# Kernel optimization log

Hardware: AMD Instinct MI355X
Metric: run time of the kernel (lower is better)

The kernel has to match this reference:

```python
import jax, jax.numpy as jnp
import numpy as np

T, B, A, OBS = 128, 16, 32, 256
K, NACT, HID = 3, 9, 32


def setup_inputs() -> dict:
    key = jax.random.key(0)
    ks = jax.random.split(key, 12)
    sc = 0.1  # small init scale for stability
    d = {}
    d["x"] = jax.random.normal(ks[0], (T, B, A, OBS), jnp.float32)
    d["done"] = jax.random.randint(ks[1], (T, B), 0, 2, jnp.int32)
    d["actions"] = jax.random.randint(ks[2], (T, B, A, K), 0, NACT, jnp.int32)
    d["W1"] = sc * jax.random.normal(ks[3], (128, OBS), jnp.float32)
    d["b1"] = jnp.zeros((128,), jnp.float32)
    d["W2"] = sc * jax.random.normal(ks[4], (128, 128), jnp.float32)
    d["b2"] = jnp.zeros((128,), jnp.float32)
    d["W3"] = sc * jax.random.normal(ks[5], (64, 128), jnp.float32)
    d["b3"] = jnp.zeros((64,), jnp.float32)
    d["Wih"] = sc * jax.random.normal(ks[6], (4 * HID, 64), jnp.float32)
    d["Whh"] = sc * jax.random.normal(ks[7], (4 * HID, HID), jnp.float32)
    d["bih"] = jnp.zeros((4 * HID,), jnp.float32)
    d["bhh"] = jnp.zeros((4 * HID,), jnp.float32)
    d["Wh"] = sc * jax.random.normal(ks[8], (K, NACT, HID), jnp.float32)
    d["bh"] = jnp.zeros((K, NACT), jnp.float32)
    d["h0"] = jnp.zeros((B * A, HID), jnp.float32)
    d["c0"] = jnp.zeros((B * A, HID), jnp.float32)
    return d


def _forward(x, done, actions, W1, b1, W2, b2, W3, b3,
             Wih, Whh, bih, bhh, Wh, bh, h0, c0):
    # MLP trunk: n_obs -> 128 -> 128 -> 64 (tanh, tanh, linear)
    z = jnp.tanh(x @ W1.T + b1)
    z = jnp.tanh(z @ W2.T + b2)
    z = z @ W3.T + b3                       # [T, B, A, 64]
    zf = z.reshape(T, B * A, 64)
    # done[t] repeated per agent (repeat_interleave along batch*agent axis)
    done_f = jnp.repeat(done.astype(x.dtype), A, axis=1)  # [T, B*A]

    def step(carry, inp):
        h, c = carry
        zt, dt = inp                        # [B*A,64], [B*A]
        mask = (1.0 - dt)[:, None]
        h = h * mask
        c = c * mask
        gates = zt @ Wih.T + bih + h @ Whh.T + bhh  # [B*A, 4H]
        i, f, g, o = jnp.split(gates, 4, axis=-1)   # PyTorch gate order i,f,g,o
        i, f, o = jax.nn.sigmoid(i), jax.nn.sigmoid(f), jax.nn.sigmoid(o)
        g = jnp.tanh(g)
        c = f * c + i * g
        h = o * jnp.tanh(c)
        return (h, c), h

    (_, _), ys = jax.lax.scan(step, (h0, c0), (zf, done_f))
    y = ys.reshape(T, B, A, HID)
    # multi-head categorical logits: stacked heads [K, NACT, HID]
    logits = jnp.einsum('tbah,knh->tbakn', y, Wh) + bh  # [T,B,A,K,NACT]
    lp = jax.nn.log_softmax(logits, axis=-1)
    entropies = -jnp.sum(jnp.exp(lp) * lp, axis=-1)     # [T,B,A,K]
    alp = jnp.take_along_axis(lp, actions[..., None], axis=-1)[..., 0]  # [T,B,A,K]
    logprobs = jnp.prod(alp, axis=-1)  # faithful: product of per-head log-probs
    return logprobs, entropies


def reference(x, done, actions, W1, b1, W2, b2, W3, b3,
              Wih, Whh, bih, bhh, Wh, bh, h0, c0):
    logprobs, entropies = _forward(x, done, actions, W1, b1, W2, b2, W3, b3,
                                   Wih, Whh, bih, bhh, Wh, bh, h0, c0)
    return actions, logprobs, entropies
```

## Files before the change

kernel.cpp:

```cpp
#include <hip/hip_runtime.h>
#include <math.h>

namespace {
constexpr int Tn = 128, Bn = 16, An = 32, OBS = 256, Kh = 3, NACT = 9, HID = 32;
constexpr int TBA = Tn * Bn * An;
constexpr int BA  = Bn * An;
constexpr int OUT_LP  = TBA * Kh;
constexpr int OUT_ENT = TBA * Kh + TBA;
constexpr int NCHUNK = 8;
constexpr int CHUNKW = Tn / NCHUNK;

constexpr int W1_OFF  = 0;
constexpr int W2_OFF  = 32768;
constexpr int W3_OFF  = 49152;
constexpr int WIH_OFF = 57344;
constexpr int W16_TOT = 65536;

typedef __fp16   pk16x2 __attribute__((ext_vector_type(2)));
typedef _Float16 half8v __attribute__((ext_vector_type(8)));
typedef float    f32x4  __attribute__((ext_vector_type(4)));
}

__device__ __forceinline__ float fast_sig(float x) {
  return __builtin_amdgcn_rcpf(1.f + __expf(-x));
}
__device__ __forceinline__ float fast_tanh(float x) {
  return fmaf(2.f, fast_sig(2.f * x), -1.f);
}
__device__ __forceinline__ unsigned h2bits(pk16x2 h) {
  return __builtin_bit_cast(unsigned, h);
}
__device__ __forceinline__ pk16x2 bits2h(unsigned u) {
  return __builtin_bit_cast(pk16x2, u);
}
__device__ __forceinline__ float dot2(pk16x2 a, pk16x2 b, float c) {
#if __has_builtin(__builtin_amdgcn_fdot2)
  return __builtin_amdgcn_fdot2(a, b, c, false);
#else
  c = fmaf((float)a.x, (float)b.x, c);
  return fmaf((float)a.y, (float)b.y, c);
#endif
}
__device__ __forceinline__ float dpp_swap1(float x) {
  return __uint_as_float((unsigned)__builtin_amdgcn_mov_dpp(
      (int)__float_as_uint(x), 0xB1, 0xF, 0xF, true));
}
__device__ __forceinline__ int first_done_ge(unsigned long long dm0,
                                             unsigned long long dm1, int n) {
  unsigned long long m0 = (n < 64) ? (dm0 & (~0ull << n)) : 0ull;
  unsigned long long m1 = (n < 64) ? dm1 : (dm1 & (~0ull << (n - 64)));
  if (m0) return __builtin_ctzll(m0);
  if (m1) return 64 + __builtin_ctzll(m1);
  return 128;
}

__global__ __launch_bounds__(256) void cvtw_act_kernel(
    const float* __restrict__ W1, const float* __restrict__ W2,
    const float* __restrict__ W3, const float* __restrict__ Wih,
    _Float16* __restrict__ w16, const int* __restrict__ actions,
    float* __restrict__ out)
{
  const int bid = blockIdx.x;
  if (bid < W16_TOT/256) {
    int i = bid * 256 + threadIdx.x;
    float v;
    if (i < W2_OFF)       v = W1[i];
    else if (i < W3_OFF)  v = W2[i - W2_OFF];
    else if (i < WIH_OFF) v = W3[i - W3_OFF];
    else                  v = Wih[i - WIH_OFF];
    w16[i] = (_Float16)v;
  } else {
    int i = (bid - W16_TOT/256) * 256 + threadIdx.x;
    out[i] = (float)actions[i];
  }
}

template<int ROWS, int WSTR>
__device__ __forceinline__ void stage_wh(const _Float16* __restrict__ Wg, int kofs,
                                         _Float16* __restrict__ wt, int tid)
{
#pragma unroll
  for (int it = 0; it < ROWS/64; ++it) {
    int idx = tid + it*512;
    int o = idx >> 3, g8 = idx & 7;
    *(half8v*)&wt[o*72 + g8*8] =
        *(const half8v*)&Wg[(size_t)o*WSTR + kofs + g8*8];
  }
}

template<int NOC, int XSTR>
__device__ __forceinline__ void mfma_slab(const _Float16* __restrict__ xsrc,
                                          const _Float16* __restrict__ wt,
                                          int rA, int ln, int quad, f32x4 acc[8])
{
#pragma unroll
  for (int kc = 0; kc < 2; ++kc) {
    half8v a = *(const half8v*)&xsrc[rA*XSTR + kc*32 + quad*8];
#pragma unroll
    for (int oc = 0; oc < NOC; ++oc) {
      half8v b = *(const half8v*)&wt[(oc*16 + ln)*72 + kc*32 + quad*8];
      acc[oc] = __builtin_amdgcn_mfma_f32_16x16x32_f16(a, b, acc[oc], 0, 0, 0);
    }
  }
}

__global__ __launch_bounds__(512) void mlp_kernel(
    const float* __restrict__ x, const _Float16* __restrict__ w16,
    const float* __restrict__ b1, const float* __restrict__ b2,
    const float* __restrict__ b3, const float* __restrict__ bih,
    const float* __restrict__ bhh, uint2* __restrict__ G1q)
{
  __shared__ __align__(16) _Float16 xs[128*72];
  __shared__ __align__(16) _Float16 wt[128*72];
  __shared__ __align__(16) _Float16 act[128*136];
  const _Float16* W1h  = w16 + W1_OFF;
  const _Float16* W2h  = w16 + W2_OFF;
  const _Float16* W3h  = w16 + W3_OFF;
  const _Float16* Wihh = w16 + WIH_OFF;
  const int tid  = threadIdx.x;
  const int w    = tid >> 6;
  const int lane = tid & 63;
  const int ln   = lane & 15;
  const int quad = lane >> 4;
  const int rA   = 16*w + ln;
  const int r0   = 16*w + quad*4;
  const int R0   = blockIdx.x * 128;
  f32x4 acc[8];

#pragma unroll
  for (int oc = 0; oc < 8; ++oc) acc[oc] = (f32x4)0.f;
  for (int kt = 0; kt < 4; ++kt) {
#pragma unroll
    for (int it = 0; it < 2; ++it) {
      int idx = tid + it*512;
      int r = idx >> 3, g8 = idx & 7;
      const float* xp = &x[(size_t)(R0 + r)*OBS + kt*64 + g8*8];
      float4 v0 = *(const float4*)xp;
      float4 v1 = *(const float4*)(xp + 4);
      half8v hv = { (_Float16)v0.x, (_Float16)v0.y, (_Float16)v0.z, (_Float16)v0.w,
                    (_Float16)v1.x, (_Float16)v1.y, (_Float16)v1.z, (_Float16)v1.w };
      *(half8v*)&xs[r*72 + g8*8] = hv;
    }
    stage_wh<128, 256>(W1h, kt*64, wt, tid);
    __syncthreads();
    mfma_slab<8, 72>(xs, wt, rA, ln, quad, acc);
    __syncthreads();
  }
#pragma unroll
  for (int oc = 0; oc < 8; ++oc) {
    int o = oc*16 + ln;
    float bv = b1[o];
#pragma unroll
    for (int r = 0; r < 4; ++r)
      act[(r0 + r)*136 + o] = (_Float16)fast_tanh(acc[oc][r] + bv);
  }

#pragma unroll
  for (int oc = 0; oc < 8; ++oc) acc[oc] = (f32x4)0.f;
  for (int kt = 0; kt < 2; ++kt) {
    stage_wh<128, 128>(W2h, kt*64, wt, tid);
    __syncthreads();
    mfma_slab<8, 136>(act + kt*64, wt, rA, ln, quad, acc);
    __syncthreads();
  }
#pragma unroll
  for (int oc = 0; oc < 8; ++oc) {
    int o = oc*16 + ln;
    float bv = b2[o];
#pragma unroll
    for (int r = 0; r < 4; ++r)
      act[(r0 + r)*136 + o] = (_Float16)fast_tanh(acc[oc][r] + bv);
  }

#pragma unroll
  for (int oc = 0; oc < 4; ++oc) acc[oc] = (f32x4)0.f;
  for (int kt = 0; kt < 2; ++kt) {
    stage_wh<64, 128>(W3h, kt*64, wt, tid);
    __syncthreads();
    mfma_slab<4, 136>(act + kt*64, wt, rA, ln, quad, acc);
    __syncthreads();
  }
#pragma unroll
  for (int oc = 0; oc < 4; ++oc) {
    int o = oc*16 + ln;
    float bv = b3[o];
#pragma unroll
    for (int r = 0; r < 4; ++r)
      xs[(r0 + r)*72 + o] = (_Float16)(acc[oc][r] + bv);
  }

#pragma unroll
  for (int oc = 0; oc < 8; ++oc) acc[oc] = (f32x4)0.f;
  stage_wh<128, 64>(Wihh, 0, wt, tid);
  __syncthreads();
  mfma_slab<8, 72>(xs, wt, rA, ln, quad, acc);
#pragma unroll
  for (int p = 0; p < 2; ++p) {
    int ui = p*16 + ln;
    float bi = bih[ui]      + bhh[ui];
    float bf = bih[ui + 32] + bhh[ui + 32];
    float bg = bih[ui + 64] + bhh[ui + 64];
    float bo = bih[ui + 96] + bhh[ui + 96];
#pragma unroll
    for (int r = 0; r < 4; ++r) {
      int n = R0 + r0 + r;
      uint2 q;
      q.x = h2bits(__builtin_amdgcn_cvt_pkrtz(acc[p  ][r] + bi, acc[p+4][r] + bg));
      q.y = h2bits(__builtin_amdgcn_cvt_pkrtz(acc[p+2][r] + bf, acc[p+6][r] + bo));
      G1q[(size_t)n*32 + ui] = q;
    }
  }
}

__global__ __launch_bounds__(64) void lstm_kernel(
    const uint2* __restrict__ G1q, const float* __restrict__ Whh,
    const int* __restrict__ done, const float* __restrict__ h0,
    const float* __restrict__ c0, unsigned* __restrict__ Y16)
{
  static_assert(BA == 512 && NCHUNK == 8, "index math below assumes 512x8");
  const int lane = threadIdx.x;
  const int u    = lane & 31;
  const int half = lane >> 5;
  const int row  = blockIdx.x & (BA - 1);
  const int ck   = blockIdx.x >> 9;
  const int b    = row >> 5;

  unsigned long long dm0 = __ballot(done[lane*Bn + b] != 0);
  unsigned long long dm1 = __ballot(done[(lane + 64)*Bn + b] != 0);

  const int s = (ck == 0) ? 0 : first_done_ge(dm0, dm1, ck * CHUNKW);
  const int e = (ck == NCHUNK - 1) ? Tn
                                   : first_done_ge(dm0, dm1, (ck + 1) * CHUNKW);
  if (s >= e) return;

  pk16x2 wA[16], wB[16];
  const int rwA = u + half*32;
#pragma unroll
  for (int k4 = 0; k4 < 8; ++k4) {
    float4 a  = *(const float4*)&Whh[(rwA     )*HID + k4*4];
    float4 bq = *(const float4*)&Whh[(rwA + 64)*HID + k4*4];
    wA[2*k4+0] = __builtin_amdgcn_cvt_pkrtz(a.x,  a.y);
    wA[2*k4+1] = __builtin_amdgcn_cvt_pkrtz(a.z,  a.w);
    wB[2*k4+0] = __builtin_amdgcn_cvt_pkrtz(bq.x, bq.y);
    wB[2*k4+1] = __builtin_amdgcn_cvt_pkrtz(bq.z, bq.w);
  }

  float c, h;
  if (ck == 0) { c = c0[row*HID + u]; h = h0[row*HID + u]; }
  else         { c = 0.f;             h = 0.f; }
  unsigned pk = h2bits(__builtin_amdgcn_cvt_pkrtz(h, dpp_swap1(h)));

  const float sSc = half ? 1.f : 2.f;
  const float m1c = half ? 1.f : 2.f;
  const float m0c = half ? 0.f : -1.f;

  const unsigned* gb = (const unsigned*)G1q + ((size_t)row*32 + u)*2 + half;
  const size_t gstride = (size_t)BA * 64;

  unsigned qcur = gb[(size_t)s * gstride];
  for (int t = s; t < e; ++t) {
    int tn = t + 1; tn = (tn < e) ? tn : (e - 1);
    unsigned qnext = gb[(size_t)tn * gstride];

    unsigned long long dbit = (t < 64) ? (dm0 >> t) : (dm1 >> (t - 64));
    float m = (dbit & 1ull) ? 0.f : 1.f;
    unsigned hp[16];
#pragma unroll
    for (int k = 0; k < 16; ++k)
      hp[k] = __builtin_amdgcn_readlane(pk, 2*k);
    float aA0 = 0.f, aA1 = 0.f, aB0 = 0.f, aB1 = 0.f;
#pragma unroll
    for (int k = 0; k < 16; k += 2) {
      pk16x2 ha = bits2h(hp[k]), hb = bits2h(hp[k+1]);
      aA0 = dot2(wA[k], ha, aA0); aA1 = dot2(wA[k+1], hb, aA1);
      aB0 = dot2(wB[k], ha, aB0); aB1 = dot2(wB[k+1], hb, aB1);
    }
    pk16x2 g2 = bits2h(qcur);
    float x0 = fmaf(m, aA0 + aA1, (float)g2.x);
    float x1 = fmaf(m, aB0 + aB1, (float)g2.y);
    float v0 = fast_sig(x0);
    float v1 = fmaf(m1c, fast_sig(sSc * x1), m0c);
    float o0 = __shfl_xor(v0, 32, 64);
    float o1 = __shfl_xor(v1, 32, 64);
    float iv = half ? o0 : v0;
    float fv = half ? v0 : o0;
    float gv = half ? o1 : v1;
    float ov = half ? v1 : o1;
    c = fmaf(fv, m * c, iv * gv);
    h = ov * fast_tanh(c);
    pk = h2bits(__builtin_amdgcn_cvt_pkrtz(h, dpp_swap1(h)));
    if ((lane & 33) == 0)
      Y16[((size_t)t*BA + row)*16 + (u >> 1)] = pk;

    qcur = qnext;
  }
}

__global__ __launch_bounds__(256) void head_kernel(
    const unsigned* __restrict__ Y16, const float* __restrict__ Wh,
    const float* __restrict__ bh, const int* __restrict__ actions,
    float* __restrict__ out)
{
  __shared__ __align__(16) float whs[27*32];
  __shared__ float bhs[32];
  const int tid = threadIdx.x;
  const int R0 = blockIdx.x * 256;
  for (int i = tid; i < 27*32; i += 256) whs[i] = Wh[i];
  if (tid < 27) bhs[tid] = bh[tid];
  const int row = R0 + tid;
  float yv[32];
#pragma unroll
  for (int i4 = 0; i4 < 4; ++i4) {
    uint4 yw = *(const uint4*)&Y16[(size_t)row*16 + i4*4];
    pk16x2 p0 = bits2h(yw.x), p1 = bits2h(yw.y), p2 = bits2h(yw.z), p3 = bits2h(yw.w);
    yv[i4*8+0] = (float)p0.x; yv[i4*8+1] = (float)p0.y;
    yv[i4*8+2] = (float)p1.x; yv[i4*8+3] = (float)p1.y;
    yv[i4*8+4] = (float)p2.x; yv[i4*8+5] = (float)p2.y;
    yv[i4*8+6] = (float)p3.x; yv[i4*8+7] = (float)p3.y;
  }
  __syncthreads();
  float l[27];
#pragma unroll
  for (int m = 0; m < 27; ++m) {
    float a = bhs[m];
#pragma unroll
    for (int k4 = 0; k4 < 8; ++k4) {
      float4 w4 = *(const float4*)&whs[m*32 + k4*4];
      a = fmaf(yv[k4*4+0], w4.x, a);
      a = fmaf(yv[k4*4+1], w4.y, a);
      a = fmaf(yv[k4*4+2], w4.z, a);
      a = fmaf(yv[k4*4+3], w4.w, a);
    }
    l[m] = a;
  }
  float logprob = 1.0f;
#pragma unroll
  for (int kk = 0; kk < 3; ++kk) {
    float mx = l[kk*9];
#pragma unroll
    for (int n = 1; n < 9; ++n) mx = fmaxf(mx, l[kk*9+n]);
    float s = 0.f;
#pragma unroll
    for (int n = 0; n < 9; ++n) s += __expf(l[kk*9+n] - mx);
    float lse = mx + __logf(s);
    float ent = 0.f;
#pragma unroll
    for (int n = 0; n < 9; ++n) {
      float lp = l[kk*9+n] - lse;
      ent -= __expf(lp) * lp;
    }
    int a = actions[row*3 + kk];
    float alp = 0.f;
#pragma unroll
    for (int n = 0; n < 9; ++n) alp = (a == n) ? (l[kk*9+n] - lse) : alp;
    logprob *= alp;
    out[OUT_ENT + row*3 + kk] = ent;
  }
  out[OUT_LP + row] = logprob;
}

extern "C" void kernel_launch(void* const* d_in, const int* in_sizes, int n_in,
                              void* d_out, int out_size, void* d_ws, size_t ws_size,
                              hipStream_t stream)
{
  const float* x       = (const float*)d_in[0];
  const int*   done    = (const int*)  d_in[1];
  const int*   actions = (const int*)  d_in[2];
  const float* W1  = (const float*)d_in[3];
  const float* b1  = (const float*)d_in[4];
  const float* W2  = (const float*)d_in[5];
  const float* b2  = (const float*)d_in[6];
  const float* W3  = (const float*)d_in[7];
  const float* b3  = (const float*)d_in[8];
  const float* Wih = (const float*)d_in[9];
  const float* Whh = (const float*)d_in[10];
  const float* bih = (const float*)d_in[11];
  const float* bhh = (const float*)d_in[12];
  const float* Wh  = (const float*)d_in[13];
  const float* bh  = (const float*)d_in[14];
  const float* h0  = (const float*)d_in[15];
  const float* c0  = (const float*)d_in[16];
  float* out = (float*)d_out;

  uint2* G1q = (uint2*)d_ws;
  unsigned* Y16 = (unsigned*)(G1q + (size_t)TBA*32);
  _Float16* W16 = (_Float16*)(Y16 + (size_t)TBA*16);

  cvtw_act_kernel<<<W16_TOT/256 + (TBA*Kh)/256, 256, 0, stream>>>(
      W1, W2, W3, Wih, W16, actions, out);
  mlp_kernel<<<TBA/128, 512, 0, stream>>>(x, W16, b1, b2, b3, bih, bhh, G1q);
  lstm_kernel<<<BA * NCHUNK, 64, 0, stream>>>(G1q, Whh, done, h0, c0, Y16);
  head_kernel<<<TBA/256, 256, 0, stream>>>(Y16, Wh, bh, actions, out);
}
```

Baseline: 172.4 us.

## Deepen LSTM gate prefetch, interleave gate lanes for DPP, double time chunks

```diff
diff --git a/kernel.cpp b/kernel.cpp
--- a/kernel.cpp
+++ b/kernel.cpp
@@ -7,7 +7,7 @@
 constexpr int BA  = Bn * An;
 constexpr int OUT_LP  = TBA * Kh;
 constexpr int OUT_ENT = TBA * Kh + TBA;
-constexpr int NCHUNK = 8;
+constexpr int NCHUNK = 16;
 constexpr int CHUNKW = Tn / NCHUNK;
 
 constexpr int W1_OFF  = 0;
@@ -44,6 +44,10 @@
 __device__ __forceinline__ float dpp_swap1(float x) {
   return __uint_as_float((unsigned)__builtin_amdgcn_mov_dpp(
       (int)__float_as_uint(x), 0xB1, 0xF, 0xF, true));
+}
+__device__ __forceinline__ float dpp_quad2(float x) {
+  return __uint_as_float((unsigned)__builtin_amdgcn_mov_dpp(
+      (int)__float_as_uint(x), 0x4E, 0xF, 0xF, true));
 }
 __device__ __forceinline__ int first_done_ge(unsigned long long dm0,
                                              unsigned long long dm1, int n) {
@@ -217,10 +221,10 @@
     const int* __restrict__ done, const float* __restrict__ h0,
     const float* __restrict__ c0, unsigned* __restrict__ Y16)
 {
-  static_assert(BA == 512 && NCHUNK == 8, "index math below assumes 512x8");
+  static_assert(BA == 512 && NCHUNK == 16, "index math below assumes 512x16");
   const int lane = threadIdx.x;
-  const int u    = lane & 31;
-  const int half = lane >> 5;
+  const int u    = lane >> 1;
+  const int half = lane & 1;
   const int row  = blockIdx.x & (BA - 1);
   const int ck   = blockIdx.x >> 9;
   const int b    = row >> 5;
@@ -248,52 +252,76 @@
   float c, h;
   if (ck == 0) { c = c0[row*HID + u]; h = h0[row*HID + u]; }
   else         { c = 0.f;             h = 0.f; }
-  unsigned pk = h2bits(__builtin_amdgcn_cvt_pkrtz(h, dpp_swap1(h)));
+  unsigned pk = h2bits(__builtin_amdgcn_cvt_pkrtz(h, dpp_quad2(h)));
 
   const float sSc = half ? 1.f : 2.f;
   const float m1c = half ? 1.f : 2.f;
   const float m0c = half ? 0.f : -1.f;
 
-  const unsigned* gb = (const unsigned*)G1q + ((size_t)row*32 + u)*2 + half;
+  const unsigned* gb = (const unsigned*)G1q + (size_t)row*64 + lane;
   const size_t gstride = (size_t)BA * 64;
 
-  unsigned qcur = gb[(size_t)s * gstride];
-  for (int t = s; t < e; ++t) {
-    int tn = t + 1; tn = (tn < e) ? tn : (e - 1);
-    unsigned qnext = gb[(size_t)tn * gstride];
-
-    unsigned long long dbit = (t < 64) ? (dm0 >> t) : (dm1 >> (t - 64));
-    float m = (dbit & 1ull) ? 0.f : 1.f;
-    unsigned hp[16];
-#pragma unroll
-    for (int k = 0; k < 16; ++k)
-      hp[k] = __builtin_amdgcn_readlane(pk, 2*k);
-    float aA0 = 0.f, aA1 = 0.f, aB0 = 0.f, aB1 = 0.f;
-#pragma unroll
-    for (int k = 0; k < 16; k += 2) {
-      pk16x2 ha = bits2h(hp[k]), hb = bits2h(hp[k+1]);
-      aA0 = dot2(wA[k], ha, aA0); aA1 = dot2(wA[k+1], hb, aA1);
-      aB0 = dot2(wB[k], ha, aB0); aB1 = dot2(wB[k+1], hb, aB1);
-    }
-    pk16x2 g2 = bits2h(qcur);
-    float x0 = fmaf(m, aA0 + aA1, (float)g2.x);
-    float x1 = fmaf(m, aB0 + aB1, (float)g2.y);
-    float v0 = fast_sig(x0);
-    float v1 = fmaf(m1c, fast_sig(sSc * x1), m0c);
-    float o0 = __shfl_xor(v0, 32, 64);
-    float o1 = __shfl_xor(v1, 32, 64);
-    float iv = half ? o0 : v0;
-    float fv = half ? v0 : o0;
-    float gv = half ? o1 : v1;
-    float ov = half ? v1 : o1;
-    c = fmaf(fv, m * c, iv * gv);
-    h = ov * fast_tanh(c);
-    pk = h2bits(__builtin_amdgcn_cvt_pkrtz(h, dpp_swap1(h)));
-    if ((lane & 33) == 0)
-      Y16[((size_t)t*BA + row)*16 + (u >> 1)] = pk;
-
-    qcur = qnext;
-  }
+  unsigned q0 = gb[(size_t)(s                      ) * gstride];
+  unsigned q1 = gb[(size_t)((s+1 < e) ? s+1 : e-1) * gstride];
+  unsigned q2 = gb[(size_t)((s+2 < e) ? s+2 : e-1) * gstride];
+  unsigned q3 = gb[(size_t)((s+3 < e) ? s+3 : e-1) * gstride];
+  unsigned q4 = gb[(size_t)((s+4 < e) ? s+4 : e-1) * gstride];
+  unsigned q5 = gb[(size_t)((s+5 < e) ? s+5 : e-1) * gstride];
+  unsigned q6 = gb[(size_t)((s+6 < e) ? s+6 : e-1) * gstride];
+  unsigned q7 = gb[(size_t)((s+7 < e) ? s+7 : e-1) * gstride];
+
+#define LSTM_PHASE(PH, Q)                                                     \
+  {                                                                           \
+    const int t = tb + (PH);                                                  \
+    unsigned cur = Q;                                                         \
+    int tpre = t + 8; tpre = (tpre < e) ? tpre : (e - 1);                     \
+    Q = gb[(size_t)tpre * gstride];                 \
+    if (t < e) {                                      \
+      unsigned long long dbit = (t < 64) ? (dm0 >> t) : (dm1 >> (t - 64));    \
+      float m = (dbit & 1ull) ? 0.f : 1.f;                                    \
+      unsigned hp[16];                                                        \
+      _Pragma("unroll") for (int k = 0; k < 16; ++k)                          \
+        hp[k] = __builtin_amdgcn_readlane(pk, 4*k);                           \
+      float aA0=0.f, aA1=0.f, aA2=0.f, aA3=0.f;                               \
+      float aB0=0.f, aB1=0.f, aB2=0.f, aB3=0.f;                               \
+      _Pragma("unroll") for (int k = 0; k < 16; k += 4) {                     \
+        pk16x2 h0v = bits2h(hp[k]),   h1v = bits2h(hp[k+1]);                  \
+        pk16x2 h2v = bits2h(hp[k+2]), h3v = bits2h(hp[k+3]);                  \
+        aA0 = dot2(wA[k],   h0v, aA0); aA1 = dot2(wA[k+1], h1v, aA1);         \
+        aA2 = dot2(wA[k+2], h2v, aA2); aA3 = dot2(wA[k+3], h3v, aA3);         \
+        aB0 = dot2(wB[k],   h0v, aB0); aB1 = dot2(wB[k+1], h1v, aB1);         \
+        aB2 = dot2(wB[k+2], h2v, aB2); aB3 = dot2(wB[k+3], h3v, aB3);         \
+      }                                                                       \
+      pk16x2 g2 = bits2h(cur);                                                \
+      float x0 = fmaf(m, (aA0 + aA1) + (aA2 + aA3), (float)g2.x);    \
+      float x1 = fmaf(m, (aB0 + aB1) + (aB2 + aB3), (float)g2.y);    \
+      float v0 = fast_sig(x0);                                                \
+      float v1 = fmaf(m1c, fast_sig(sSc * x1), m0c);                          \
+      float o0 = dpp_swap1(v0);                   \
+      float o1 = dpp_swap1(v1);                                               \
+      float iv = half ? o0 : v0;                                              \
+      float fv = half ? v0 : o0;                                              \
+      float gv = half ? o1 : v1;                                              \
+      float ov = half ? v1 : o1;                                              \
+      c = fmaf(fv, m * c, iv * gv);                                           \
+      h = ov * fast_tanh(c);                                                  \
+      pk = h2bits(__builtin_amdgcn_cvt_pkrtz(h, dpp_quad2(h)));               \
+      if ((lane & 3) == 0)                                                    \
+        Y16[((size_t)t*BA + row)*16 + (lane >> 2)] = pk;                      \
+    }                                                                         \
+  }
+
+  for (int tb = s; tb < e; tb += 8) {
+    LSTM_PHASE(0, q0)
+    LSTM_PHASE(1, q1)
+    LSTM_PHASE(2, q2)
+    LSTM_PHASE(3, q3)
+    LSTM_PHASE(4, q4)
+    LSTM_PHASE(5, q5)
+    LSTM_PHASE(6, q6)
+    LSTM_PHASE(7, q7)
+  }
+#undef LSTM_PHASE
 }
 
 __global__ __launch_bounds__(256) void head_kernel(
```

Measured after the change: 171.7 us. Within noise of the previous version (-0.4%).

## Use MFMA for LSTM recurrence over 16-row groups with finer time chunks

Applied to the files above, without the earlier changes.

```diff
diff --git a/kernel.cpp b/kernel.cpp
--- a/kernel.cpp
+++ b/kernel.cpp
@@ -7,7 +7,7 @@
 constexpr int BA  = Bn * An;
 constexpr int OUT_LP  = TBA * Kh;
 constexpr int OUT_ENT = TBA * Kh + TBA;
-constexpr int NCHUNK = 8;
+constexpr int NCHUNK = 32;
 constexpr int CHUNKW = Tn / NCHUNK;
 
 constexpr int W1_OFF  = 0;
@@ -32,18 +32,6 @@
 }
 __device__ __forceinline__ pk16x2 bits2h(unsigned u) {
   return __builtin_bit_cast(pk16x2, u);
-}
-__device__ __forceinline__ float dot2(pk16x2 a, pk16x2 b, float c) {
-#if __has_builtin(__builtin_amdgcn_fdot2)
-  return __builtin_amdgcn_fdot2(a, b, c, false);
-#else
-  c = fmaf((float)a.x, (float)b.x, c);
-  return fmaf((float)a.y, (float)b.y, c);
-#endif
-}
-__device__ __forceinline__ float dpp_swap1(float x) {
-  return __uint_as_float((unsigned)__builtin_amdgcn_mov_dpp(
-      (int)__float_as_uint(x), 0xB1, 0xF, 0xF, true));
 }
 __device__ __forceinline__ int first_done_ge(unsigned long long dm0,
                                              unsigned long long dm1, int n) {
@@ -57,12 +45,14 @@
 __global__ __launch_bounds__(256) void cvtw_act_kernel(
     const float* __restrict__ W1, const float* __restrict__ W2,
     const float* __restrict__ W3, const float* __restrict__ Wih,
-    _Float16* __restrict__ w16, const int* __restrict__ actions,
-    float* __restrict__ out)
+    _Float16* __restrict__ w16, const float* __restrict__ Whh,
+    const int* __restrict__ done, _Float16* __restrict__ wt16,
+    unsigned long long* __restrict__ dmask)
 {
   const int bid = blockIdx.x;
+  const int tid = threadIdx.x;
   if (bid < W16_TOT/256) {
-    int i = bid * 256 + threadIdx.x;
+    int i = bid * 256 + tid;
     float v;
     if (i < W2_OFF)       v = W1[i];
     else if (i < W3_OFF)  v = W2[i - W2_OFF];
@@ -70,8 +60,20 @@
     else                  v = Wih[i - WIH_OFF];
     w16[i] = (_Float16)v;
   } else {
-    int i = (bid - W16_TOT/256) * 256 + threadIdx.x;
-    out[i] = (float)actions[i];
+    for (int i = tid; i < 4096; i += 256) {
+      int tl = i >> 9, rem = i & 511, l = rem >> 3, j = rem & 7;
+      int gate = 16*tl + (l & 15);
+      int unit = ((l >> 4) << 3) + j;
+      wt16[i] = (_Float16)Whh[gate*HID + unit];
+    }
+    if (tid < 64) {
+#pragma unroll
+      for (int b = 0; b < Bn; ++b) {
+        unsigned long long m0 = __ballot(done[tid*Bn + b] != 0);
+        unsigned long long m1 = __ballot(done[(tid + 64)*Bn + b] != 0);
+        if (tid == 0) { dmask[2*b] = m0; dmask[2*b + 1] = m1; }
+      }
+    }
   }
 }
 
@@ -213,87 +215,161 @@
 }
 
 __global__ __launch_bounds__(64) void lstm_kernel(
-    const uint2* __restrict__ G1q, const float* __restrict__ Whh,
-    const int* __restrict__ done, const float* __restrict__ h0,
-    const float* __restrict__ c0, unsigned* __restrict__ Y16)
-{
-  static_assert(BA == 512 && NCHUNK == 8, "index math below assumes 512x8");
+    const uint2* __restrict__ G1q, const _Float16* __restrict__ wt16,
+    const unsigned long long* __restrict__ dmask,
+    const float* __restrict__ h0, const float* __restrict__ c0,
+    unsigned* __restrict__ Y16)
+{
+  static_assert(BA == 512 && NCHUNK == 32, "index math below assumes 512x32");
   const int lane = threadIdx.x;
-  const int u    = lane & 31;
-  const int half = lane >> 5;
-  const int row  = blockIdx.x & (BA - 1);
-  const int ck   = blockIdx.x >> 9;
-  const int b    = row >> 5;
-
-  unsigned long long dm0 = __ballot(done[lane*Bn + b] != 0);
-  unsigned long long dm1 = __ballot(done[(lane + 64)*Bn + b] != 0);
+  const int ln   = lane & 15;
+  const int q    = lane >> 4;
+  const int rg   = blockIdx.x & 31;
+  const int ck   = blockIdx.x >> 5;
+  const int R0   = rg * 16;
+  const int b    = R0 >> 5;
+
+  const unsigned long long dm0 = dmask[2*b];
+  const unsigned long long dm1 = dmask[2*b + 1];
 
   const int s = (ck == 0) ? 0 : first_done_ge(dm0, dm1, ck * CHUNKW);
   const int e = (ck == NCHUNK - 1) ? Tn
                                    : first_done_ge(dm0, dm1, (ck + 1) * CHUNKW);
   if (s >= e) return;
 
-  pk16x2 wA[16], wB[16];
-  const int rwA = u + half*32;
-#pragma unroll
-  for (int k4 = 0; k4 < 8; ++k4) {
-    float4 a  = *(const float4*)&Whh[(rwA     )*HID + k4*4];
-    float4 bq = *(const float4*)&Whh[(rwA + 64)*HID + k4*4];
-    wA[2*k4+0] = __builtin_amdgcn_cvt_pkrtz(a.x,  a.y);
-    wA[2*k4+1] = __builtin_amdgcn_cvt_pkrtz(a.z,  a.w);
-    wB[2*k4+0] = __builtin_amdgcn_cvt_pkrtz(bq.x, bq.y);
-    wB[2*k4+1] = __builtin_amdgcn_cvt_pkrtz(bq.z, bq.w);
-  }
-
-  float c, h;
-  if (ck == 0) { c = c0[row*HID + u]; h = h0[row*HID + u]; }
-  else         { c = 0.f;             h = 0.f; }
-  unsigned pk = h2bits(__builtin_amdgcn_cvt_pkrtz(h, dpp_swap1(h)));
-
-  const float sSc = half ? 1.f : 2.f;
-  const float m1c = half ? 1.f : 2.f;
-  const float m0c = half ? 0.f : -1.f;
-
-  const unsigned* gb = (const unsigned*)G1q + ((size_t)row*32 + u)*2 + half;
-  const size_t gstride = (size_t)BA * 64;
-
-  unsigned qcur = gb[(size_t)s * gstride];
+  half8v wA0 = *(const half8v*)&wt16[0*512 + lane*8];
+  half8v wA1 = *(const half8v*)&wt16[1*512 + lane*8];
+  half8v wA2 = *(const half8v*)&wt16[2*512 + lane*8];
+  half8v wA3 = *(const half8v*)&wt16[3*512 + lane*8];
+  half8v wA4 = *(const half8v*)&wt16[4*512 + lane*8];
+  half8v wA5 = *(const half8v*)&wt16[5*512 + lane*8];
+  half8v wA6 = *(const half8v*)&wt16[6*512 + lane*8];
+  half8v wA7 = *(const half8v*)&wt16[7*512 + lane*8];
+
+  const float4 z4 = {0.f, 0.f, 0.f, 0.f};
+  float4 cs0, cs1;
+  unsigned w0, w1, w2, w3;
+  if (ck == 0) {
+    const float* hp = &h0[(size_t)(R0 + ln)*HID + 4*q];
+    const float* cp = &c0[(size_t)(R0 + ln)*HID + 4*q];
+    float4 ha = *(const float4*)hp;
+    float4 hb = *(const float4*)(hp + 16);
+    cs0 = *(const float4*)cp;
+    cs1 = *(const float4*)(cp + 16);
+    w0 = h2bits(__builtin_amdgcn_cvt_pkrtz(ha.x, ha.y));
+    w1 = h2bits(__builtin_amdgcn_cvt_pkrtz(ha.z, ha.w));
+    w2 = h2bits(__builtin_amdgcn_cvt_pkrtz(hb.x, hb.y));
+    w3 = h2bits(__builtin_amdgcn_cvt_pkrtz(hb.z, hb.w));
+  } else {
+    cs0 = z4; cs1 = z4;
+    w0 = w1 = w2 = w3 = 0u;
+  }
+
+  const int aA = (ln + ((q & 1) << 5)) << 2;
+  const int aB = aA + (16 << 2);
+  const bool loq = (q < 2);
+
+  const uint2* gb = G1q + ((size_t)(R0 + ln) * 32 + 4*q);
+  const size_t gstep = (size_t)BA * 32;
+
+#define LOADG(T, A0, A1, A2, A3)                                  \
+  { const uint2* p_ = gb + (size_t)(T) * gstep;                   \
+    A0 = *(const uint4*)(p_);      A1 = *(const uint4*)(p_ + 2);  \
+    A2 = *(const uint4*)(p_ + 16); A3 = *(const uint4*)(p_ + 18); }
+
+  uint4 rc0, rc1, rc2, rc3;
+  LOADG(s, rc0, rc1, rc2, rc3);
+
   for (int t = s; t < e; ++t) {
-    int tn = t + 1; tn = (tn < e) ? tn : (e - 1);
-    unsigned qnext = gb[(size_t)tn * gstride];
+    int tn = (t + 1 < e) ? t + 1 : e - 1;
+    uint4 rn0, rn1, rn2, rn3;
+    LOADG(tn, rn0, rn1, rn2, rn3);
 
     unsigned long long dbit = (t < 64) ? (dm0 >> t) : (dm1 >> (t - 64));
-    float m = (dbit & 1ull) ? 0.f : 1.f;
-    unsigned hp[16];
-#pragma unroll
-    for (int k = 0; k < 16; ++k)
-      hp[k] = __builtin_amdgcn_readlane(pk, 2*k);
-    float aA0 = 0.f, aA1 = 0.f, aB0 = 0.f, aB1 = 0.f;
-#pragma unroll
-    for (int k = 0; k < 16; k += 2) {
-      pk16x2 ha = bits2h(hp[k]), hb = bits2h(hp[k+1]);
-      aA0 = dot2(wA[k], ha, aA0); aA1 = dot2(wA[k+1], hb, aA1);
-      aB0 = dot2(wB[k], ha, aB0); aB1 = dot2(wB[k+1], hb, aB1);
-    }
-    pk16x2 g2 = bits2h(qcur);
-    float x0 = fmaf(m, aA0 + aA1, (float)g2.x);
-    float x1 = fmaf(m, aB0 + aB1, (float)g2.y);
-    float v0 = fast_sig(x0);
-    float v1 = fmaf(m1c, fast_sig(sSc * x1), m0c);
-    float o0 = __shfl_xor(v0, 32, 64);
-    float o1 = __shfl_xor(v1, 32, 64);
-    float iv = half ? o0 : v0;
-    float fv = half ? v0 : o0;
-    float gv = half ? o1 : v1;
-    float ov = half ? v1 : o1;
-    c = fmaf(fv, m * c, iv * gv);
-    h = ov * fast_tanh(c);
-    pk = h2bits(__builtin_amdgcn_cvt_pkrtz(h, dpp_swap1(h)));
-    if ((lane & 33) == 0)
-      Y16[((size_t)t*BA + row)*16 + (u >> 1)] = pk;
-
-    qcur = qnext;
-  }
+    unsigned b0, b1, b2, b3;
+    if (dbit & 1ull) {
+      b0 = b1 = b2 = b3 = 0u;
+      cs0 = z4; cs1 = z4;
+    } else {
+      unsigned e0 = (unsigned)__builtin_amdgcn_ds_bpermute(aA, (int)w0);
+      unsigned e1 = (unsigned)__builtin_amdgcn_ds_bpermute(aA, (int)w1);
+      unsigned e2 = (unsigned)__builtin_amdgcn_ds_bpermute(aA, (int)w2);
+      unsigned e3 = (unsigned)__builtin_amdgcn_ds_bpermute(aA, (int)w3);
+      unsigned o0 = (unsigned)__builtin_amdgcn_ds_bpermute(aB, (int)w0);
+      unsigned o1 = (unsigned)__builtin_amdgcn_ds_bpermute(aB, (int)w1);
+      unsigned o2 = (unsigned)__builtin_amdgcn_ds_bpermute(aB, (int)w2);
+      unsigned o3 = (unsigned)__builtin_amdgcn_ds_bpermute(aB, (int)w3);
+      b0 = loq ? e0 : e2;  b1 = loq ? e1 : e3;
+      b2 = loq ? o0 : o2;  b3 = loq ? o1 : o3;
+    }
+    uint4 bu; bu.x = b0; bu.y = b1; bu.z = b2; bu.w = b3;
+    half8v B = __builtin_bit_cast(half8v, bu);
+
+    f32x4 ci0, cf0, cg0, co0, ci1, cf1, cg1, co1;
+    {
+      pk16x2 ig, fo;
+      ig = bits2h(rc0.x); fo = bits2h(rc0.y);
+      ci0[0] = ig.x; cg0[0] = ig.y; cf0[0] = fo.x; co0[0] = fo.y;
+      ig = bits2h(rc0.z); fo = bits2h(rc0.w);
+      ci0[1] = ig.x; cg0[1] = ig.y; cf0[1] = fo.x; co0[1] = fo.y;
+      ig = bits2h(rc1.x); fo = bits2h(rc1.y);
+      ci0[2] = ig.x; cg0[2] = ig.y; cf0[2] = fo.x; co0[2] = fo.y;
+      ig = bits2h(rc1.z); fo = bits2h(rc1.w);
+      ci0[3] = ig.x; cg0[3] = ig.y; cf0[3] = fo.x; co0[3] = fo.y;
+      ig = bits2h(rc2.x); fo = bits2h(rc2.y);
+      ci1[0] = ig.x; cg1[0] = ig.y; cf1[0] = fo.x; co1[0] = fo.y;
+      ig = bits2h(rc2.z); fo = bits2h(rc2.w);
+      ci1[1] = ig.x; cg1[1] = ig.y; cf1[1] = fo.x; co1[1] = fo.y;
+      ig = bits2h(rc3.x); fo = bits2h(rc3.y);
+      ci1[2] = ig.x; cg1[2] = ig.y; cf1[2] = fo.x; co1[2] = fo.y;
+      ig = bits2h(rc3.z); fo = bits2h(rc3.w);
+      ci1[3] = ig.x; cg1[3] = ig.y; cf1[3] = fo.x; co1[3] = fo.y;
+    }
+
+    f32x4 ai0 = __builtin_amdgcn_mfma_f32_16x16x32_f16(wA0, B, ci0, 0, 0, 0);
+    f32x4 ai1 = __builtin_amdgcn_mfma_f32_16x16x32_f16(wA1, B, ci1, 0, 0, 0);
+    f32x4 af0 = __builtin_amdgcn_mfma_f32_16x16x32_f16(wA2, B, cf0, 0, 0, 0);
+    f32x4 af1 = __builtin_amdgcn_mfma_f32_16x16x32_f16(wA3, B, cf1, 0, 0, 0);
+    f32x4 ag0 = __builtin_amdgcn_mfma_f32_16x16x32_f16(wA4, B, cg0, 0, 0, 0);
+    f32x4 ag1 = __builtin_amdgcn_mfma_f32_16x16x32_f16(wA5, B, cg1, 0, 0, 0);
+    f32x4 ao0 = __builtin_amdgcn_mfma_f32_16x16x32_f16(wA6, B, co0, 0, 0, 0);
+    f32x4 ao1 = __builtin_amdgcn_mfma_f32_16x16x32_f16(wA7, B, co1, 0, 0, 0);
+
+    f32x4 hva, hvb;
+#pragma unroll
+    for (int r = 0; r < 4; ++r) {
+      float iv = fast_sig(ai0[r]);
+      float fv = fast_sig(af0[r]);
+      float gv = fast_tanh(ag0[r]);
+      float ov = fast_sig(ao0[r]);
+      float cc = fmaf(fv, cs0[r], iv * gv);
+      cs0[r] = cc;
+      hva[r] = ov * fast_tanh(cc);
+    }
+#pragma unroll
+    for (int r = 0; r < 4; ++r) {
+      float iv = fast_sig(ai1[r]);
+      float fv = fast_sig(af1[r]);
+      float gv = fast_tanh(ag1[r]);
+      float ov = fast_sig(ao1[r]);
+      float cc = fmaf(fv, cs1[r], iv * gv);
+      cs1[r] = cc;
+      hvb[r] = ov * fast_tanh(cc);
+    }
+
+    w0 = h2bits(__builtin_amdgcn_cvt_pkrtz(hva[0], hva[1]));
+    w1 = h2bits(__builtin_amdgcn_cvt_pkrtz(hva[2], hva[3]));
+    w2 = h2bits(__builtin_amdgcn_cvt_pkrtz(hvb[0], hvb[1]));
+    w3 = h2bits(__builtin_amdgcn_cvt_pkrtz(hvb[2], hvb[3]));
+    unsigned* yb = &Y16[((size_t)t*BA + R0 + ln)*16 + 2*q];
+    uint2 ya; ya.x = w0; ya.y = w1;
+    uint2 yc; yc.x = w2; yc.y = w3;
+    *(uint2*)yb       = ya;
+    *(uint2*)(yb + 8) = yc;
+
+    rc0 = rn0; rc1 = rn1; rc2 = rn2; rc3 = rn3;
+  }
+#undef LOADG
 }
 
 __global__ __launch_bounds__(256) void head_kernel(
@@ -350,6 +426,7 @@
       ent -= __expf(lp) * lp;
     }
     int a = actions[row*3 + kk];
+    out[row*3 + kk] = (float)a;
     float alp = 0.f;
 #pragma unroll
     for (int n = 0; n < 9; ++n) alp = (a == n) ? (l[kk*9+n] - lse) : alp;
@@ -385,10 +462,12 @@
   uint2* G1q = (uint2*)d_ws;
   unsigned* Y16 = (unsigned*)(G1q + (size_t)TBA*32);
   _Float16* W16 = (_Float16*)(Y16 + (size_t)TBA*16);
-
-  cvtw_act_kernel<<<W16_TOT/256 + (TBA*Kh)/256, 256, 0, stream>>>(
-      W1, W2, W3, Wih, W16, actions, out);
+  _Float16* WT16 = W16 + W16_TOT;
+  unsigned long long* Dm = (unsigned long long*)(WT16 + 4096);
+
+  cvtw_act_kernel<<<W16_TOT/256 + 1, 256, 0, stream>>>(
+      W1, W2, W3, Wih, W16, Whh, done, WT16, Dm);
   mlp_kernel<<<TBA/128, 512, 0, stream>>>(x, W16, b1, b2, b3, bih, bhh, G1q);
-  lstm_kernel<<<BA * NCHUNK, 64, 0, stream>>>(G1q, Whh, done, h0, c0, Y16);
+  lstm_kernel<<<32 * NCHUNK, 64, 0, stream>>>(G1q, WT16, Dm, h0, c0, Y16);
   head_kernel<<<TBA/256, 256, 0, stream>>>(Y16, Wh, bh, actions, out);
 }
```

Result: faster. 168.0 us (-2.6%).
